# Performance work log

Hardware: AMD Instinct MI355X
Metric: run time of the kernel (lower is better)

Reference implementation:

```python
import jax, jax.numpy as jnp
import numpy as np

COS_EPS = 1e-8    # torch.nn.CosineSimilarity default eps
NORM_EPS = 1e-12  # torch F.normalize default eps


def _cosine_gram(x, y):
    # Pairwise cosine similarity as a GEMM over row-normalized vectors,
    # matching torch: dot / max(|x|*|y|, eps). Avoids O(b^2*d) broadcast.
    dots = x @ y.T                               # [b, b]
    nx = jnp.linalg.norm(x, axis=1)              # [b]
    ny = jnp.linalg.norm(y, axis=1)              # [b]
    return dots / jnp.maximum(nx[:, None] * ny[None, :], COS_EPS)


def _row_normalize(g):
    # torch F.normalize(p=2, dim=1): x / max(||x||, eps)
    n = jnp.linalg.norm(g, axis=1, keepdims=True)
    return g / jnp.maximum(n, NORM_EPS)


def setup_inputs() -> dict:
    key = jax.random.key(0)
    k1, k2, k3, k4 = jax.random.split(key, 4)
    bsz, dim = 8192, 128
    return {
        "zxs": jax.random.normal(k1, (bsz, dim), dtype=jnp.float32),
        "zys": jax.random.normal(k2, (bsz, dim), dtype=jnp.float32),
        "zxt": jax.random.normal(k3, (bsz, dim), dtype=jnp.float32),
        "zyt": jax.random.normal(k4, (bsz, dim), dtype=jnp.float32),
        "temperature": jnp.asarray(0.5, dtype=jnp.float32),
    }


def reference(zxs, zys, zxt, zyt, temperature):
    bsz = zxs.shape[0]
    sim_s = _row_normalize(_cosine_gram(zxs, zys) / temperature)  # [b, b]
    sim_t = _row_normalize(_cosine_gram(zxt, zyt) / temperature)  # [b, b]
    g_diff = sim_t - sim_s
    loss = jnp.sum(g_diff * g_diff) / (bsz * bsz)
    return loss
```

## Files before the change

kernel.cpp:

```cpp
#include <hip/hip_runtime.h>
#include <hip/hip_bf16.h>


typedef __attribute__((ext_vector_type(8))) short short8;
typedef __attribute__((ext_vector_type(4))) float float4v;

#define BSZ 8192
#define DIM 128
#define NP  64
#define INV_B2 1.4901161193847656e-08f

__device__ __forceinline__ short f2bf(float x) {
    union { __hip_bfloat16 b; short s; } u;
    u.b = __float2bfloat16(x);
    return u.s;
}

__global__ __launch_bounds__(256) void prep(
    const float* __restrict__ Yt, const float* __restrict__ Ys,
    short* __restrict__ YT, float* __restrict__ out)
{
    __shared__ float rsum[2][64];
    __shared__ float invn[64];

    const int tid   = threadIdx.x;
    const int lane  = tid & 63;
    const int wave  = tid >> 6;
    const int d     = tid & 127;
    const int khalf = tid >> 7;
    const int chunk = blockIdx.x;
    const int mat   = blockIdx.y;
    const float* Y  = mat ? Ys : Yt;

    if (chunk == 0 && mat == 0 && tid == 0) out[0] = 0.f;

    float v[32];
    const float* base = Y + (size_t)(chunk * 64 + khalf * 32) * DIM + d;
    #pragma unroll
    for (int i = 0; i < 32; ++i) v[i] = base[(size_t)i * DIM];

    #pragma unroll
    for (int i = 0; i < 32; ++i) {
        float ss = v[i] * v[i];
        #pragma unroll
        for (int off = 1; off < 64; off <<= 1) ss += __shfl_xor(ss, off);
        if (lane == 0) rsum[wave & 1][khalf * 32 + i] = ss;
    }
    __syncthreads();
    if (tid < 64) {
        float s = rsum[0][tid] + rsum[1][tid];
        invn[tid] = (s > 0.f) ? rsqrtf(s) : 0.f;
    }
    __syncthreads();

    short* yt = YT + ((size_t)mat * 128 + d) * BSZ + chunk * 64 + khalf * 32;
    #pragma unroll
    for (int g = 0; g < 4; ++g) {
        short8 pk;
        #pragma unroll
        for (int j = 0; j < 8; ++j) {
            int i = g * 8 + j;
            pk[j] = f2bf(v[i] * invn[khalf * 32 + i]);
        }
        *(short8*)&yt[g * 8] = pk;
    }
}

__global__ __launch_bounds__(512) void gram_g(
    const short* __restrict__ YT, float* __restrict__ partial)
{
    const int tid  = threadIdx.x;
    const int lane = tid & 63;
    const int s1   = tid >> 6;
    const int q    = lane >> 4;
    const int l15  = lane & 15;
    const int split = blockIdx.x;
    const int gram  = blockIdx.y;

    const short* Ta = (gram == 1) ? YT + (size_t)128 * BSZ : YT;
    const short* Tb = (gram == 0) ? YT : YT + (size_t)128 * BSZ;
    const int k0 = split * 128;

    float4v acc[8];
    #pragma unroll
    for (int s2 = 0; s2 < 8; ++s2) acc[s2] = (float4v){0.f, 0.f, 0.f, 0.f};

    #pragma unroll
    for (int kk = 0; kk < 4; ++kk) {
        const int ko = k0 + kk * 32 + q * 8;
        short8 fa = *(const short8*)&Ta[(size_t)(s1 * 16 + l15) * BSZ + ko];
        short8 fb[8];
        #pragma unroll
        for (int s2 = 0; s2 < 8; ++s2)
            fb[s2] = *(const short8*)&Tb[(size_t)(s2 * 16 + l15) * BSZ + ko];
        #pragma unroll
        for (int s2 = 0; s2 < 8; ++s2)
            acc[s2] = __builtin_amdgcn_mfma_f32_16x16x32_bf16(fa, fb[s2], acc[s2], 0, 0, 0);
    }

    float* P = partial + ((size_t)(gram * NP + split) << 14);
    #pragma unroll
    for (int s2 = 0; s2 < 8; ++s2)
        #pragma unroll
        for (int r = 0; r < 4; ++r)
            P[((s1 * 16 + q * 4 + r) << 7) + s2 * 16 + l15] = acc[s2][r];
}

__global__ __launch_bounds__(256) void reduce_g(
    const float* __restrict__ partial, __hip_bfloat16* __restrict__ Gb)
{
    int o = blockIdx.x * 256 + threadIdx.x;
    int g = o >> 14, rem = o & 16383;
    float s = 0.f;
    for (int b = 0; b < NP; ++b)
        s += partial[((size_t)(g * NP + b) << 14) + rem];
    int d1 = rem >> 7, d2 = rem & 127;
    Gb[(g << 14) + (d2 << 7) + d1] = __float2bfloat16(s);
}

__global__ __launch_bounds__(256) void quad_k(
    const float* __restrict__ Xt, const float* __restrict__ Xs,
    const __hip_bfloat16* __restrict__ Gb, float* __restrict__ out)
{
    const int tid  = threadIdx.x;
    const int lane = tid & 63;
    const int wave = tid >> 6;
    const int q    = lane >> 4;
    const int l15  = lane & 15;
    const int rbase = blockIdx.x * 64 + wave * 16;

    short8 At[4], As[4];
    #pragma unroll
    for (int kk = 0; kk < 4; ++kk) {
        const float* pt = Xt + (size_t)(rbase + l15) * DIM + kk * 32 + q * 8;
        const float* ps = Xs + (size_t)(rbase + l15) * DIM + kk * 32 + q * 8;
        float4 t0 = *(const float4*)pt, t1 = *(const float4*)(pt + 4);
        float4 s0 = *(const float4*)ps, s1 = *(const float4*)(ps + 4);
        short8 a, b;
        a[0]=f2bf(t0.x); a[1]=f2bf(t0.y); a[2]=f2bf(t0.z); a[3]=f2bf(t0.w);
        a[4]=f2bf(t1.x); a[5]=f2bf(t1.y); a[6]=f2bf(t1.z); a[7]=f2bf(t1.w);
        b[0]=f2bf(s0.x); b[1]=f2bf(s0.y); b[2]=f2bf(s0.z); b[3]=f2bf(s0.w);
        b[4]=f2bf(s1.x); b[5]=f2bf(s1.y); b[6]=f2bf(s1.z); b[7]=f2bf(s1.w);
        At[kk] = a; As[kk] = b;
    }

    float fA[4] = {0,0,0,0}, fB[4] = {0,0,0,0}, fC[4] = {0,0,0,0};
    const short* G = (const short*)Gb;

    #pragma unroll
    for (int nt = 0; nt < 8; ++nt) {
        int d2 = nt * 16 + l15;
        float4v qt = {0.f,0.f,0.f,0.f}, qs = qt, qc = qt;
        #pragma unroll
        for (int kk = 0; kk < 4; ++kk) {
            int off = (d2 << 7) + kk * 32 + q * 8;
            short8 Bt = *(const short8*)&G[off];
            short8 Bs = *(const short8*)&G[16384 + off];
            short8 Bm = *(const short8*)&G[32768 + off];
            qt = __builtin_amdgcn_mfma_f32_16x16x32_bf16(At[kk], Bt, qt, 0, 0, 0);
            qs = __builtin_amdgcn_mfma_f32_16x16x32_bf16(As[kk], Bs, qs, 0, 0, 0);
            qc = __builtin_amdgcn_mfma_f32_16x16x32_bf16(At[kk], Bm, qc, 0, 0, 0);
        }
        #pragma unroll
        for (int r = 0; r < 4; ++r) {
            int row = rbase + q * 4 + r;
            float xtv = Xt[(size_t)row * DIM + d2];
            float xsv = Xs[(size_t)row * DIM + d2];
            fA[r] += qt[r] * xtv;
            fB[r] += qs[r] * xsv;
            fC[r] += qc[r] * xsv;
        }
    }

    float wl = 0.f;
    #pragma unroll
    for (int r = 0; r < 4; ++r) {
        float A = fA[r], B = fB[r], C = fC[r];
        #pragma unroll
        for (int off = 1; off < 16; off <<= 1) {
            A += __shfl_xor(A, off);
            B += __shfl_xor(B, off);
            C += __shfl_xor(C, off);
        }
        float contrib = 2.f - 2.f * C * rsqrtf(A * B);
        wl += (l15 == 0) ? contrib : 0.f;
    }
    wl += __shfl_xor(wl, 16);
    wl += __shfl_xor(wl, 32);

    __shared__ float wred[4];
    if (lane == 0) wred[wave] = wl;
    __syncthreads();
    if (tid == 0)
        atomicAdd(out, (wred[0] + wred[1] + wred[2] + wred[3]) * INV_B2);
}

extern "C" void kernel_launch(void* const* d_in, const int* in_sizes, int n_in,
                              void* d_out, int out_size, void* d_ws, size_t ws_size,
                              hipStream_t stream) {
    const float* zxs = (const float*)d_in[0];
    const float* zys = (const float*)d_in[1];
    const float* zxt = (const float*)d_in[2];
    const float* zyt = (const float*)d_in[3];
    float* out = (float*)d_out;

    char* ws = (char*)d_ws;
    short* YT = (short*)ws;
    float* partial = (float*)(ws + (size_t)4 * 1024 * 1024);
    __hip_bfloat16* Gb = (__hip_bfloat16*)(ws + (size_t)4 * 1024 * 1024
                                              + (size_t)3 * NP * 16384 * sizeof(float));

    prep    <<<dim3(128, 2), 256, 0, stream>>>(zyt, zys, YT, out);
    gram_g  <<<dim3(NP, 3),  512, 0, stream>>>(YT, partial);
    reduce_g<<<192,          256, 0, stream>>>(partial, Gb);
    quad_k  <<<128,          256, 0, stream>>>(zxt, zxs, Gb, out);
}
```

Before: 109.1 us.

## Fuse four kernels into one cooperative kernel with grid syncs and bf16 partials

```diff
diff --git a/kernel.cpp b/kernel.cpp
--- a/kernel.cpp
+++ b/kernel.cpp
@@ -1,5 +1,8 @@
 #include <hip/hip_runtime.h>
 #include <hip/hip_bf16.h>
+#include <hip/hip_cooperative_groups.h>
+
+namespace cg = cooperative_groups;
 
 
 typedef __attribute__((ext_vector_type(8))) short short8;
@@ -15,184 +18,194 @@
     u.b = __float2bfloat16(x);
     return u.s;
 }
-
-__global__ __launch_bounds__(256) void prep(
+__device__ __forceinline__ float bf2f(short s) {
+    union { unsigned int u; float f; } v;
+    v.u = ((unsigned int)(unsigned short)s) << 16;
+    return v.f;
+}
+
+__global__ void __launch_bounds__(256, 1) fused(
     const float* __restrict__ Yt, const float* __restrict__ Ys,
-    short* __restrict__ YT, float* __restrict__ out)
+    const float* __restrict__ Xt, const float* __restrict__ Xs,
+    short* __restrict__ YT,
+    short* __restrict__ partial,
+    short* __restrict__ Gb,
+    float* __restrict__ out)
 {
-    __shared__ float rsum[2][64];
-    __shared__ float invn[64];
-
-    const int tid   = threadIdx.x;
-    const int lane  = tid & 63;
-    const int wave  = tid >> 6;
-    const int d     = tid & 127;
-    const int khalf = tid >> 7;
-    const int chunk = blockIdx.x;
-    const int mat   = blockIdx.y;
-    const float* Y  = mat ? Ys : Yt;
-
-    if (chunk == 0 && mat == 0 && tid == 0) out[0] = 0.f;
-
-    float v[32];
-    const float* base = Y + (size_t)(chunk * 64 + khalf * 32) * DIM + d;
-    #pragma unroll
-    for (int i = 0; i < 32; ++i) v[i] = base[(size_t)i * DIM];
-
-    #pragma unroll
-    for (int i = 0; i < 32; ++i) {
-        float ss = v[i] * v[i];
-        #pragma unroll
-        for (int off = 1; off < 64; off <<= 1) ss += __shfl_xor(ss, off);
-        if (lane == 0) rsum[wave & 1][khalf * 32 + i] = ss;
-    }
-    __syncthreads();
-    if (tid < 64) {
-        float s = rsum[0][tid] + rsum[1][tid];
-        invn[tid] = (s > 0.f) ? rsqrtf(s) : 0.f;
-    }
-    __syncthreads();
-
-    short* yt = YT + ((size_t)mat * 128 + d) * BSZ + chunk * 64 + khalf * 32;
-    #pragma unroll
-    for (int g = 0; g < 4; ++g) {
-        short8 pk;
-        #pragma unroll
-        for (int j = 0; j < 8; ++j) {
-            int i = g * 8 + j;
-            pk[j] = f2bf(v[i] * invn[khalf * 32 + i]);
-        }
-        *(short8*)&yt[g * 8] = pk;
-    }
-}
-
-__global__ __launch_bounds__(512) void gram_g(
-    const short* __restrict__ YT, float* __restrict__ partial)
-{
-    const int tid  = threadIdx.x;
-    const int lane = tid & 63;
-    const int s1   = tid >> 6;
-    const int q    = lane >> 4;
-    const int l15  = lane & 15;
-    const int split = blockIdx.x;
-    const int gram  = blockIdx.y;
-
-    const short* Ta = (gram == 1) ? YT + (size_t)128 * BSZ : YT;
-    const short* Tb = (gram == 0) ? YT : YT + (size_t)128 * BSZ;
-    const int k0 = split * 128;
-
-    float4v acc[8];
-    #pragma unroll
-    for (int s2 = 0; s2 < 8; ++s2) acc[s2] = (float4v){0.f, 0.f, 0.f, 0.f};
-
-    #pragma unroll
-    for (int kk = 0; kk < 4; ++kk) {
-        const int ko = k0 + kk * 32 + q * 8;
-        short8 fa = *(const short8*)&Ta[(size_t)(s1 * 16 + l15) * BSZ + ko];
-        short8 fb[8];
-        #pragma unroll
-        for (int s2 = 0; s2 < 8; ++s2)
-            fb[s2] = *(const short8*)&Tb[(size_t)(s2 * 16 + l15) * BSZ + ko];
-        #pragma unroll
-        for (int s2 = 0; s2 < 8; ++s2)
-            acc[s2] = __builtin_amdgcn_mfma_f32_16x16x32_bf16(fa, fb[s2], acc[s2], 0, 0, 0);
-    }
-
-    float* P = partial + ((size_t)(gram * NP + split) << 14);
-    #pragma unroll
-    for (int s2 = 0; s2 < 8; ++s2)
-        #pragma unroll
-        for (int r = 0; r < 4; ++r)
-            P[((s1 * 16 + q * 4 + r) << 7) + s2 * 16 + l15] = acc[s2][r];
-}
-
-__global__ __launch_bounds__(256) void reduce_g(
-    const float* __restrict__ partial, __hip_bfloat16* __restrict__ Gb)
-{
-    int o = blockIdx.x * 256 + threadIdx.x;
-    int g = o >> 14, rem = o & 16383;
-    float s = 0.f;
-    for (int b = 0; b < NP; ++b)
-        s += partial[((size_t)(g * NP + b) << 14) + rem];
-    int d1 = rem >> 7, d2 = rem & 127;
-    Gb[(g << 14) + (d2 << 7) + d1] = __float2bfloat16(s);
-}
-
-__global__ __launch_bounds__(256) void quad_k(
-    const float* __restrict__ Xt, const float* __restrict__ Xs,
-    const __hip_bfloat16* __restrict__ Gb, float* __restrict__ out)
-{
+    cg::grid_group grid = cg::this_grid();
+
     const int tid  = threadIdx.x;
     const int lane = tid & 63;
     const int wave = tid >> 6;
     const int q    = lane >> 4;
     const int l15  = lane & 15;
-    const int rbase = blockIdx.x * 64 + wave * 16;
-
-    short8 At[4], As[4];
-    #pragma unroll
-    for (int kk = 0; kk < 4; ++kk) {
-        const float* pt = Xt + (size_t)(rbase + l15) * DIM + kk * 32 + q * 8;
-        const float* ps = Xs + (size_t)(rbase + l15) * DIM + kk * 32 + q * 8;
-        float4 t0 = *(const float4*)pt, t1 = *(const float4*)(pt + 4);
-        float4 s0 = *(const float4*)ps, s1 = *(const float4*)(ps + 4);
-        short8 a, b;
-        a[0]=f2bf(t0.x); a[1]=f2bf(t0.y); a[2]=f2bf(t0.z); a[3]=f2bf(t0.w);
-        a[4]=f2bf(t1.x); a[5]=f2bf(t1.y); a[6]=f2bf(t1.z); a[7]=f2bf(t1.w);
-        b[0]=f2bf(s0.x); b[1]=f2bf(s0.y); b[2]=f2bf(s0.z); b[3]=f2bf(s0.w);
-        b[4]=f2bf(s1.x); b[5]=f2bf(s1.y); b[6]=f2bf(s1.z); b[7]=f2bf(s1.w);
-        At[kk] = a; As[kk] = b;
-    }
-
-    float fA[4] = {0,0,0,0}, fB[4] = {0,0,0,0}, fC[4] = {0,0,0,0};
-    const short* G = (const short*)Gb;
-
-    #pragma unroll
-    for (int nt = 0; nt < 8; ++nt) {
-        int d2 = nt * 16 + l15;
-        float4v qt = {0.f,0.f,0.f,0.f}, qs = qt, qc = qt;
+    const int bid  = blockIdx.x;
+
+    {
+        __shared__ float rsum[2][64];
+        __shared__ float invn[64];
+        const int d     = tid & 127;
+        const int khalf = tid >> 7;
+        const int chunk = bid & 127;
+        const int mat   = bid >> 7;
+        const float* Y  = mat ? Ys : Yt;
+
+        if (bid == 0 && tid == 0) out[0] = 0.f;
+
+        float v[32];
+        const float* base = Y + (size_t)(chunk * 64 + khalf * 32) * DIM + d;
+        #pragma unroll
+        for (int i = 0; i < 32; ++i) v[i] = base[(size_t)i * DIM];
+
+        #pragma unroll
+        for (int i = 0; i < 32; ++i) {
+            float ss = v[i] * v[i];
+            #pragma unroll
+            for (int off = 1; off < 64; off <<= 1) ss += __shfl_xor(ss, off);
+            if (lane == 0) rsum[wave & 1][khalf * 32 + i] = ss;
+        }
+        __syncthreads();
+        if (tid < 64) {
+            float s = rsum[0][tid] + rsum[1][tid];
+            invn[tid] = (s > 0.f) ? rsqrtf(s) : 0.f;
+        }
+        __syncthreads();
+
+        short* yt = YT + ((size_t)mat * 128 + d) * BSZ + chunk * 64 + khalf * 32;
+        #pragma unroll
+        for (int g = 0; g < 4; ++g) {
+            short8 pk;
+            #pragma unroll
+            for (int j = 0; j < 8; ++j) {
+                int i = g * 8 + j;
+                pk[j] = f2bf(v[i] * invn[khalf * 32 + i]);
+            }
+            *(short8*)&yt[g * 8] = pk;
+        }
+    }
+    __threadfence();
+    grid.sync();
+
+    for (int u = bid; u < 384; u += 256) {
+        const int split = u & 63;
+        const int rest  = u >> 6;
+        const int gram  = rest >> 1;
+        const int half  = rest & 1;
+        const int s1    = half * 4 + wave;
+
+        const short* Ta = (gram == 1) ? YT + (size_t)128 * BSZ : YT;
+        const short* Tb = (gram == 0) ? YT : YT + (size_t)128 * BSZ;
+        const int k0 = split * 128;
+
+        float4v acc[8];
+        #pragma unroll
+        for (int s2 = 0; s2 < 8; ++s2) acc[s2] = (float4v){0.f, 0.f, 0.f, 0.f};
+
         #pragma unroll
         for (int kk = 0; kk < 4; ++kk) {
-            int off = (d2 << 7) + kk * 32 + q * 8;
-            short8 Bt = *(const short8*)&G[off];
-            short8 Bs = *(const short8*)&G[16384 + off];
-            short8 Bm = *(const short8*)&G[32768 + off];
-            qt = __builtin_amdgcn_mfma_f32_16x16x32_bf16(At[kk], Bt, qt, 0, 0, 0);
-            qs = __builtin_amdgcn_mfma_f32_16x16x32_bf16(As[kk], Bs, qs, 0, 0, 0);
-            qc = __builtin_amdgcn_mfma_f32_16x16x32_bf16(At[kk], Bm, qc, 0, 0, 0);
-        }
+            const int ko = k0 + kk * 32 + q * 8;
+            short8 fa = *(const short8*)&Ta[(size_t)(s1 * 16 + l15) * BSZ + ko];
+            short8 fb[8];
+            #pragma unroll
+            for (int s2 = 0; s2 < 8; ++s2)
+                fb[s2] = *(const short8*)&Tb[(size_t)(s2 * 16 + l15) * BSZ + ko];
+            #pragma unroll
+            for (int s2 = 0; s2 < 8; ++s2)
+                acc[s2] = __builtin_amdgcn_mfma_f32_16x16x32_bf16(fa, fb[s2], acc[s2], 0, 0, 0);
+        }
+
+        short* P = partial + ((size_t)(gram * NP + split) << 14);
+        #pragma unroll
+        for (int s2 = 0; s2 < 8; ++s2)
+            #pragma unroll
+            for (int r = 0; r < 4; ++r)
+                P[((s1 * 16 + q * 4 + r) << 7) + s2 * 16 + l15] = f2bf(acc[s2][r]);
+    }
+    __threadfence();
+    grid.sync();
+
+    {
+        int o = bid * 256 + tid;
+        if (o < 3 * 16384) {
+            int g = o >> 14, rem = o & 16383;
+            const short* P = partial + ((size_t)(g * NP) << 14) + rem;
+            float s = 0.f;
+            #pragma unroll 8
+            for (int b = 0; b < NP; ++b) s += bf2f(P[(size_t)b << 14]);
+            int d1 = rem >> 7, d2 = rem & 127;
+            Gb[(g << 14) + (d2 << 7) + d1] = f2bf(s);
+        }
+    }
+    __threadfence();
+    grid.sync();
+
+    if (bid < 128) {
+        const int rbase = bid * 64 + wave * 16;
+
+        short8 At[4], As[4];
+        #pragma unroll
+        for (int kk = 0; kk < 4; ++kk) {
+            const float* pt = Xt + (size_t)(rbase + l15) * DIM + kk * 32 + q * 8;
+            const float* ps = Xs + (size_t)(rbase + l15) * DIM + kk * 32 + q * 8;
+            float4 t0 = *(const float4*)pt, t1 = *(const float4*)(pt + 4);
+            float4 s0 = *(const float4*)ps, s1 = *(const float4*)(ps + 4);
+            short8 a, b;
+            a[0]=f2bf(t0.x); a[1]=f2bf(t0.y); a[2]=f2bf(t0.z); a[3]=f2bf(t0.w);
+            a[4]=f2bf(t1.x); a[5]=f2bf(t1.y); a[6]=f2bf(t1.z); a[7]=f2bf(t1.w);
+            b[0]=f2bf(s0.x); b[1]=f2bf(s0.y); b[2]=f2bf(s0.z); b[3]=f2bf(s0.w);
+            b[4]=f2bf(s1.x); b[5]=f2bf(s1.y); b[6]=f2bf(s1.z); b[7]=f2bf(s1.w);
+            At[kk] = a; As[kk] = b;
+        }
+
+        float fA[4] = {0,0,0,0}, fB[4] = {0,0,0,0}, fC[4] = {0,0,0,0};
+
+        #pragma unroll
+        for (int nt = 0; nt < 8; ++nt) {
+            int d2 = nt * 16 + l15;
+            float4v qt = {0.f,0.f,0.f,0.f}, qs = qt, qc = qt;
+            #pragma unroll
+            for (int kk = 0; kk < 4; ++kk) {
+                int off = (d2 << 7) + kk * 32 + q * 8;
+                short8 Bt = *(const short8*)&Gb[off];
+                short8 Bs = *(const short8*)&Gb[16384 + off];
+                short8 Bm = *(const short8*)&Gb[32768 + off];
+                qt = __builtin_amdgcn_mfma_f32_16x16x32_bf16(At[kk], Bt, qt, 0, 0, 0);
+                qs = __builtin_amdgcn_mfma_f32_16x16x32_bf16(As[kk], Bs, qs, 0, 0, 0);
+                qc = __builtin_amdgcn_mfma_f32_16x16x32_bf16(At[kk], Bm, qc, 0, 0, 0);
+            }
+            #pragma unroll
+            for (int r = 0; r < 4; ++r) {
+                int row = rbase + q * 4 + r;
+                float xtv = Xt[(size_t)row * DIM + d2];
+                float xsv = Xs[(size_t)row * DIM + d2];
+                fA[r] += qt[r] * xtv;
+                fB[r] += qs[r] * xsv;
+                fC[r] += qc[r] * xsv;
+            }
+        }
+
+        float wl = 0.f;
         #pragma unroll
         for (int r = 0; r < 4; ++r) {
-            int row = rbase + q * 4 + r;
-            float xtv = Xt[(size_t)row * DIM + d2];
-            float xsv = Xs[(size_t)row * DIM + d2];
-            fA[r] += qt[r] * xtv;
-            fB[r] += qs[r] * xsv;
-            fC[r] += qc[r] * xsv;
-        }
-    }
-
-    float wl = 0.f;
-    #pragma unroll
-    for (int r = 0; r < 4; ++r) {
-        float A = fA[r], B = fB[r], C = fC[r];
-        #pragma unroll
-        for (int off = 1; off < 16; off <<= 1) {
-            A += __shfl_xor(A, off);
-            B += __shfl_xor(B, off);
-            C += __shfl_xor(C, off);
-        }
-        float contrib = 2.f - 2.f * C * rsqrtf(A * B);
-        wl += (l15 == 0) ? contrib : 0.f;
-    }
-    wl += __shfl_xor(wl, 16);
-    wl += __shfl_xor(wl, 32);
-
-    __shared__ float wred[4];
-    if (lane == 0) wred[wave] = wl;
-    __syncthreads();
-    if (tid == 0)
-        atomicAdd(out, (wred[0] + wred[1] + wred[2] + wred[3]) * INV_B2);
+            float A = fA[r], B = fB[r], C = fC[r];
+            #pragma unroll
+            for (int off = 1; off < 16; off <<= 1) {
+                A += __shfl_xor(A, off);
+                B += __shfl_xor(B, off);
+                C += __shfl_xor(C, off);
+            }
+            float contrib = 2.f - 2.f * C * rsqrtf(A * B);
+            wl += (l15 == 0) ? contrib : 0.f;
+        }
+        wl += __shfl_xor(wl, 16);
+        wl += __shfl_xor(wl, 32);
+
+        __shared__ float wred[4];
+        if (lane == 0) wred[wave] = wl;
+        __syncthreads();
+        if (tid == 0)
+            atomicAdd(out, (wred[0] + wred[1] + wred[2] + wred[3]) * INV_B2);
+    }
 }
 
 extern "C" void kernel_launch(void* const* d_in, const int* in_sizes, int n_in,
@@ -205,13 +218,12 @@
     float* out = (float*)d_out;
 
     char* ws = (char*)d_ws;
-    short* YT = (short*)ws;
-    float* partial = (float*)(ws + (size_t)4 * 1024 * 1024);
-    __hip_bfloat16* Gb = (__hip_bfloat16*)(ws + (size_t)4 * 1024 * 1024
-                                              + (size_t)3 * NP * 16384 * sizeof(float));
-
-    prep    <<<dim3(128, 2), 256, 0, stream>>>(zyt, zys, YT, out);
-    gram_g  <<<dim3(NP, 3),  512, 0, stream>>>(YT, partial);
-    reduce_g<<<192,          256, 0, stream>>>(partial, Gb);
-    quad_k  <<<128,          256, 0, stream>>>(zxt, zxs, Gb, out);
-}
+    short* YT      = (short*)ws;
+    short* partial = (short*)(ws + (size_t)4  * 1024 * 1024);
+    short* Gb      = (short*)(ws + (size_t)11 * 1024 * 1024);
+
+    void* args[] = {(void*)&zyt, (void*)&zys, (void*)&zxt, (void*)&zxs,
+                    (void*)&YT, (void*)&partial, (void*)&Gb, (void*)&out};
+    hipLaunchCooperativeKernel((const void*)fused, dim3(256), dim3(256),
+                               args, 0, stream);
+}
```

Measured after the change: 295.4 us. 2.71x slower.
